# Performance work log

Measured on AMD Instinct MI355X. Metric: run time of the kernel, lower is better.

Reference implementation:

```python
import jax, jax.numpy as jnp
import numpy as np

DIM = 1024
NUM_HEADS = 16
HEAD_DIM = DIM // NUM_HEADS


def setup_inputs() -> dict:
    key = jax.random.key(0)
    k1, k2, k3 = jax.random.split(key, 3)
    x = jax.random.normal(k1, (4, 1024, DIM), dtype=jnp.float32)
    # match nn.Linear init scale roughly: small weights
    Wqkv = jax.random.normal(k2, (3 * DIM, DIM), dtype=jnp.float32) * (1.0 / np.sqrt(DIM))
    Wproj = jax.random.normal(k3, (DIM, DIM), dtype=jnp.float32) * (1.0 / np.sqrt(DIM))
    bproj = jnp.zeros((DIM,), dtype=jnp.float32)
    return {"x": x, "Wqkv": Wqkv, "Wproj": Wproj, "bproj": bproj}


def reference(x, Wqkv, Wproj, bproj):
    bsz, tsz, chans = x.shape
    # fused QKV projection (qkv_bias=False): [B,T,3C]
    qkv = jnp.einsum("btc,oc->bto", x, Wqkv)
    qkv = qkv.reshape(bsz, tsz, 3, NUM_HEADS, HEAD_DIM)
    q = qkv[:, :, 0].transpose(0, 2, 1, 3)  # [B,H,T,D]
    k = qkv[:, :, 1].transpose(0, 2, 1, 3)
    v = qkv[:, :, 2].transpose(0, 2, 1, 3)
    scale = 1.0 / np.sqrt(HEAD_DIM)
    logits = jnp.einsum("bhqd,bhkd->bhqk", q, k) * scale  # [B,H,T,T]
    attn = jax.nn.softmax(logits, axis=-1)
    out = jnp.einsum("bhqk,bhkd->bhqd", attn, v)  # [B,H,T,D]
    out = out.transpose(0, 2, 1, 3).reshape(bsz, tsz, chans)
    return jnp.einsum("btc,oc->bto", out, Wproj) + bproj
```

## Files before the change

### kernel.cpp

```cpp
#include <hip/hip_runtime.h>
#include <hip/hip_bf16.h>

typedef __attribute__((ext_vector_type(8))) short bfrag8;
typedef __attribute__((ext_vector_type(4))) short bfrag4;
typedef __attribute__((ext_vector_type(4))) float floatx4;

typedef unsigned short ushort_t;
typedef unsigned int uint_t;
typedef unsigned long long u64_t;

static __device__ __forceinline__ uint_t pk_bf16(float a, float b) {
    union { __hip_bfloat162 h; uint_t u; } cv;
    cv.h = __float22bfloat162_rn(make_float2(a, b));
    return cv.u;
}

#if __has_builtin(__builtin_amdgcn_mfma_f32_16x16x16_bf16)
static __device__ __forceinline__ floatx4 mfma16(bfrag4 a, bfrag4 b, floatx4 c) {
    return __builtin_amdgcn_mfma_f32_16x16x16_bf16(a, b, c, 0, 0, 0);
}
#elif __has_builtin(__builtin_amdgcn_mfma_f32_16x16x16bf16_1k)
static __device__ __forceinline__ floatx4 mfma16(bfrag4 a, bfrag4 b, floatx4 c) {
    return __builtin_amdgcn_mfma_f32_16x16x16bf16_1k(a, b, c, 0, 0, 0);
}
#else
static __device__ __forceinline__ floatx4 mfma16(bfrag4 a, bfrag4 b, floatx4 c) {
    bfrag8 az = {a[0], 0, a[1], 0, a[2], 0, a[3], 0};
    bfrag8 bz = {b[0], 0, b[1], 0, b[2], 0, b[3], 0};
    return __builtin_amdgcn_mfma_f32_16x16x32_bf16(az, bz, c, 0, 0, 0);
}
#endif

static __device__ __forceinline__ void gl_lds16(const ushort_t* g, ushort_t* l) {
    __builtin_amdgcn_global_load_lds(
        (const __attribute__((address_space(1))) void*)g,
        (__attribute__((address_space(3))) void*)l, 16, 0, 0);
}

__global__ __launch_bounds__(256)
void cvt_all(const float* __restrict__ x, const float* __restrict__ wqkv,
             const float* __restrict__ wproj, ushort_t* __restrict__ xb,
             ushort_t* __restrict__ wqkvb, ushort_t* __restrict__ wprojb) {
    int blk = blockIdx.x;
    const float* src; ushort_t* dst; int base;
    if (blk < 4096)      { src = x;     dst = xb;     base = blk; }
    else if (blk < 7168) { src = wqkv;  dst = wqkvb;  base = blk - 4096; }
    else                 { src = wproj; dst = wprojb; base = blk - 7168; }
    int i = (base * 256 + threadIdx.x) * 4;
    float4 f = *(const float4*)(src + i);
    uint_t lo = pk_bf16(f.x, f.y);
    uint_t hi = pk_bf16(f.z, f.w);
    uint2 u = {lo, hi};
    *(uint2*)(dst + i) = u;
}

__global__ __launch_bounds__(256, 3)
void qkv_gemm(const ushort_t* __restrict__ A, const ushort_t* __restrict__ B,
              ushort_t* __restrict__ qp, ushort_t* __restrict__ kp,
              ushort_t* __restrict__ vTp) {
    const int K = 1024;
    __shared__ ushort_t As[128 * 64];
    __shared__ ushort_t Bs[128 * 64];
    int tid = threadIdx.x;
    int wave = __builtin_amdgcn_readfirstlane(tid >> 6);
    int lane = tid & 63;
    int quad = lane >> 4, l16 = lane & 15;
    int wm = (wave >> 1) * 64, wn = (wave & 1) * 64;
    int m0 = blockIdx.y * 128, n0 = blockIdx.x * 128;

    int rl = lane >> 3;
    int gc = (lane & 7) ^ rl;

    floatx4 acc[4][4] = {};

    const ushort_t* Ag = A + (size_t)m0 * K;
    const ushort_t* Bg = B + (size_t)n0 * K;

    for (int k0 = 0; k0 < K; k0 += 64) {
        __syncthreads();
#pragma unroll
        for (int i = 0; i < 4; i++) {
            int row = wave * 32 + i * 8 + rl;
            gl_lds16(Ag + (size_t)row * K + k0 + gc * 8, &As[(wave * 32 + i * 8) * 64]);
            gl_lds16(Bg + (size_t)row * K + k0 + gc * 8, &Bs[(wave * 32 + i * 8) * 64]);
        }
        __syncthreads();
#pragma unroll
        for (int ks = 0; ks < 2; ks++) {
            bfrag8 af[4], bf[4];
#pragma unroll
            for (int mt = 0; mt < 4; mt++) {
                int r = wm + mt * 16 + l16;
                af[mt] = *(const bfrag8*)&As[r * 64 + ((4 * ks + quad) ^ (r & 7)) * 8];
            }
#pragma unroll
            for (int nt = 0; nt < 4; nt++) {
                int r = wn + nt * 16 + l16;
                bf[nt] = *(const bfrag8*)&Bs[r * 64 + ((4 * ks + quad) ^ (r & 7)) * 8];
            }
#pragma unroll
            for (int mt = 0; mt < 4; mt++)
#pragma unroll
                for (int nt = 0; nt < 4; nt++)
                    acc[mt][nt] = __builtin_amdgcn_mfma_f32_16x16x32_bf16(
                        af[mt], bf[nt], acc[mt][nt], 0, 0, 0);
        }
    }

    int s = n0 >> 10;
    if (s < 2) {
        ushort_t* dst = (s == 0) ? qp : kp;
        float scl = (s == 0) ? 0.125f : 1.0f;
#pragma unroll
        for (int mt = 0; mt < 4; mt++) {
#pragma unroll
            for (int nt = 0; nt < 4; nt++) {
                int o = (n0 & 1023) + wn + nt * 16 + l16;
                int h = o >> 6, d = o & 63;
                uint_t p01 = pk_bf16(acc[mt][nt][0] * scl, acc[mt][nt][1] * scl);
                uint_t p23 = pk_bf16(acc[mt][nt][2] * scl, acc[mt][nt][3] * scl);
                ushort_t pv[4] = {(ushort_t)p01, (ushort_t)(p01 >> 16),
                                  (ushort_t)p23, (ushort_t)(p23 >> 16)};
#pragma unroll
                for (int r = 0; r < 4; r++) {
                    int t = m0 + wm + mt * 16 + quad * 4 + r;
                    int b = t >> 10, tt = t & 1023;
                    dst[((size_t)(b * 16 + h) * 1024 + tt) * 64 + d] = pv[r];
                }
            }
        }
    } else {
#pragma unroll
        for (int mt = 0; mt < 4; mt++) {
            int t = m0 + wm + mt * 16 + quad * 4;
            int b = t >> 10, tt = t & 1023;
#pragma unroll
            for (int nt = 0; nt < 4; nt++) {
                int o = (n0 & 1023) + wn + nt * 16 + l16;
                int h = o >> 6, d = o & 63;
                uint_t p01 = pk_bf16(acc[mt][nt][0], acc[mt][nt][1]);
                uint_t p23 = pk_bf16(acc[mt][nt][2], acc[mt][nt][3]);
                u64_t pk = ((u64_t)p23 << 32) | p01;
                *(u64_t*)&vTp[((size_t)(b * 16 + h) * 64 + d) * 1024 + tt] = pk;
            }
        }
    }
}

__global__ __launch_bounds__(256, 2)
void attn_kernel(const ushort_t* __restrict__ q, const ushort_t* __restrict__ k,
                 const ushort_t* __restrict__ vT, ushort_t* __restrict__ out) {
    int id = blockIdx.x;
    int bh = (id & 7) + ((id >> 6) << 3);
    int qt = (id >> 3) & 7;
    const ushort_t* qb = q + (size_t)bh * 1024 * 64;
    const ushort_t* kb = k + (size_t)bh * 1024 * 64;
    const ushort_t* vtb = vT + (size_t)bh * 64 * 1024;
    int tid = threadIdx.x;
    int wave = __builtin_amdgcn_readfirstlane(tid >> 6);
    int lane = tid & 63;
    int quad = lane >> 4, l16 = lane & 15;
    int q0 = qt * 128 + wave * 32;

    __shared__ ushort_t Ks[128 * 64];
    __shared__ ushort_t VTs[64 * 132];

    int rl = lane >> 3;
    int gc = (lane & 7) ^ rl;

    bfrag8 qf[2][2];
#pragma unroll
    for (int mt = 0; mt < 2; mt++)
#pragma unroll
        for (int ks = 0; ks < 2; ks++)
            qf[mt][ks] = *(const bfrag8*)&qb[(size_t)(q0 + mt * 16 + l16) * 64 + ks * 32 + quad * 8];

    floatx4 oacc[2][4] = {};
    float li[2] = {0.f, 0.f};

    int vd = tid >> 2;
    int vc = tid & 3;

    for (int kt = 0; kt < 8; kt++) {
        uint4 vv[4];
#pragma unroll
        for (int i = 0; i < 4; i++)
            vv[i] = *(const uint4*)&vtb[(size_t)vd * 1024 + kt * 128 + (vc + i * 4) * 8];
        __syncthreads();
#pragma unroll
        for (int i = 0; i < 4; i++) {
            int row = wave * 32 + i * 8 + rl;
            gl_lds16(kb + (size_t)(kt * 128 + row) * 64 + gc * 8, &Ks[(wave * 32 + i * 8) * 64]);
        }
#pragma unroll
        for (int i = 0; i < 4; i++)
            *(uint4*)&VTs[vd * 132 + (vc + i * 4) * 8] = vv[i];
        __syncthreads();

#pragma unroll
        for (int half = 0; half < 2; half++) {
            floatx4 st[2][4] = {};
#pragma unroll
            for (int ks = 0; ks < 2; ks++) {
                bfrag8 kf[4];
#pragma unroll
                for (int tt = 0; tt < 4; tt++) {
                    int r = (half * 4 + tt) * 16 + l16;
                    kf[tt] = *(const bfrag8*)&Ks[r * 64 + ((4 * ks + quad) ^ (r & 7)) * 8];
                }
#pragma unroll
                for (int mt = 0; mt < 2; mt++)
#pragma unroll
                    for (int tt = 0; tt < 4; tt++)
                        st[mt][tt] = __builtin_amdgcn_mfma_f32_16x16x32_bf16(
                            kf[tt], qf[mt][ks], st[mt][tt], 0, 0, 0);
            }

            bfrag4 pf[2][4];
#pragma unroll
            for (int mt = 0; mt < 2; mt++)
#pragma unroll
                for (int tt = 0; tt < 4; tt++) {
                    float p0 = __expf(st[mt][tt][0]);
                    float p1 = __expf(st[mt][tt][1]);
                    float p2 = __expf(st[mt][tt][2]);
                    float p3 = __expf(st[mt][tt][3]);
                    li[mt] += (p0 + p1) + (p2 + p3);
                    union { uint2 u; bfrag4 f; } pk;
                    pk.u.x = pk_bf16(p0, p1);
                    pk.u.y = pk_bf16(p2, p3);
                    pf[mt][tt] = pk.f;
                }

#pragma unroll
            for (int tt = 0; tt < 4; tt++) {
                int keyoff = (half * 4 + tt) * 16;
                bfrag4 vb[4];
#pragma unroll
                for (int nd = 0; nd < 4; nd++)
                    vb[nd] = *(const bfrag4*)&VTs[(nd * 16 + l16) * 132 + keyoff + quad * 4];
#pragma unroll
                for (int mt = 0; mt < 2; mt++)
#pragma unroll
                    for (int nd = 0; nd < 4; nd++)
                        oacc[mt][nd] = mfma16(pf[mt][tt], vb[nd], oacc[mt][nd]);
            }
        }
    }

    float inv[2][4];
#pragma unroll
    for (int mt = 0; mt < 2; mt++) {
        float s0 = li[mt];
        s0 += __shfl_xor(s0, 16);
        s0 += __shfl_xor(s0, 32);
#pragma unroll
        for (int r = 0; r < 4; r++)
            inv[mt][r] = 1.0f / __shfl(s0, quad * 4 + r);
    }

    int b = bh >> 4, h = bh & 15;
#pragma unroll
    for (int mt = 0; mt < 2; mt++)
#pragma unroll
        for (int nd = 0; nd < 4; nd++) {
            uint_t c01 = pk_bf16(oacc[mt][nd][0] * inv[mt][0], oacc[mt][nd][1] * inv[mt][1]);
            uint_t c23 = pk_bf16(oacc[mt][nd][2] * inv[mt][2], oacc[mt][nd][3] * inv[mt][3]);
            ushort_t pv[4] = {(ushort_t)c01, (ushort_t)(c01 >> 16),
                              (ushort_t)c23, (ushort_t)(c23 >> 16)};
#pragma unroll
            for (int r = 0; r < 4; r++) {
                int t = q0 + mt * 16 + quad * 4 + r;
                int c = h * 64 + nd * 16 + l16;
                out[((size_t)(b * 1024 + t)) * 1024 + c] = pv[r];
            }
        }
}

__global__ __launch_bounds__(256, 2)
void proj_gemm(const ushort_t* __restrict__ A, const ushort_t* __restrict__ B,
               const float* __restrict__ bias, float* __restrict__ out) {
    const int K = 1024;
    __shared__ ushort_t As[64 * 64];
    __shared__ ushort_t Bs[128 * 64];
    int tid = threadIdx.x;
    int wave = __builtin_amdgcn_readfirstlane(tid >> 6);
    int lane = tid & 63;
    int quad = lane >> 4, l16 = lane & 15;
    int wm = (wave >> 1) * 32, wn = (wave & 1) * 64;
    int m0 = blockIdx.y * 64, n0 = blockIdx.x * 128;

    int rl = lane >> 3;
    int gc = (lane & 7) ^ rl;

    floatx4 acc[2][4] = {};

    const ushort_t* Ag = A + (size_t)m0 * K;
    const ushort_t* Bg = B + (size_t)n0 * K;

    for (int k0 = 0; k0 < K; k0 += 64) {
        __syncthreads();
#pragma unroll
        for (int i = 0; i < 2; i++) {
            int row = wave * 16 + i * 8 + rl;
            gl_lds16(Ag + (size_t)row * K + k0 + gc * 8, &As[(wave * 16 + i * 8) * 64]);
        }
#pragma unroll
        for (int i = 0; i < 4; i++) {
            int row = wave * 32 + i * 8 + rl;
            gl_lds16(Bg + (size_t)row * K + k0 + gc * 8, &Bs[(wave * 32 + i * 8) * 64]);
        }
        __syncthreads();
#pragma unroll
        for (int ks = 0; ks < 2; ks++) {
            bfrag8 af[2], bf[4];
#pragma unroll
            for (int mt = 0; mt < 2; mt++) {
                int r = wm + mt * 16 + l16;
                af[mt] = *(const bfrag8*)&As[r * 64 + ((4 * ks + quad) ^ (r & 7)) * 8];
            }
#pragma unroll
            for (int nt = 0; nt < 4; nt++) {
                int r = wn + nt * 16 + l16;
                bf[nt] = *(const bfrag8*)&Bs[r * 64 + ((4 * ks + quad) ^ (r & 7)) * 8];
            }
#pragma unroll
            for (int mt = 0; mt < 2; mt++)
#pragma unroll
                for (int nt = 0; nt < 4; nt++)
                    acc[mt][nt] = __builtin_amdgcn_mfma_f32_16x16x32_bf16(
                        af[mt], bf[nt], acc[mt][nt], 0, 0, 0);
        }
    }

#pragma unroll
    for (int mt = 0; mt < 2; mt++) {
#pragma unroll
        for (int nt = 0; nt < 4; nt++) {
            int o = n0 + wn + nt * 16 + l16;
            float bv = bias[o];
#pragma unroll
            for (int r = 0; r < 4; r++) {
                int t = m0 + wm + mt * 16 + quad * 4 + r;
                out[(size_t)t * 1024 + o] = acc[mt][nt][r] + bv;
            }
        }
    }
}

extern "C" void kernel_launch(void* const* d_in, const int* in_sizes, int n_in,
                              void* d_out, int out_size, void* d_ws, size_t ws_size,
                              hipStream_t stream) {
    const float* x     = (const float*)d_in[0];
    const float* Wqkv  = (const float*)d_in[1];
    const float* Wproj = (const float*)d_in[2];
    const float* bproj = (const float*)d_in[3];
    float* out = (float*)d_out;

    char* ws = (char*)d_ws;
    ushort_t* xb     = (ushort_t*)(ws);
    ushort_t* wqkvb  = (ushort_t*)(ws + ((size_t)8 << 20));
    ushort_t* wprojb = (ushort_t*)(ws + ((size_t)14 << 20));
    ushort_t* qp     = (ushort_t*)(ws + ((size_t)16 << 20));
    ushort_t* kp     = (ushort_t*)(ws + ((size_t)24 << 20));
    ushort_t* vTp    = (ushort_t*)(ws + ((size_t)40 << 20));
    ushort_t* attn   = (ushort_t*)(ws + ((size_t)48 << 20));

    cvt_all<<<8192, 256, 0, stream>>>(x, Wqkv, Wproj, xb, wqkvb, wprojb);
    qkv_gemm<<<dim3(24, 32), 256, 0, stream>>>(xb, wqkvb, qp, kp, vTp);
    attn_kernel<<<512, 256, 0, stream>>>(qp, kp, vTp, attn);
    proj_gemm<<<dim3(8, 64), 256, 0, stream>>>(attn, wprojb, bproj, out);
}
```

Measured before the change: 157.9 us.

## Switch GEMMs to 32x32x16 MFMA and add XCD-aware block swizzle

Both the QKV and output-projection GEMMs move from 16x16x32 MFMA tiles to 32x32x16 MFMA tiles. This halves the number of LDS fragment loads per MFMA and uses the denser instruction. The launch grids become 1D, with block indices remapped so that consecutive blocks on the same XCD share M rows for better L2 reuse. The epilogues are rewritten for the 32x32 accumulator layout, and the per-element scatter stores stay in place.

```diff
diff --git a/kernel.cpp b/kernel.cpp
--- a/kernel.cpp
+++ b/kernel.cpp
@@ -4,6 +4,7 @@
 typedef __attribute__((ext_vector_type(8))) short bfrag8;
 typedef __attribute__((ext_vector_type(4))) short bfrag4;
 typedef __attribute__((ext_vector_type(4))) float floatx4;
+typedef __attribute__((ext_vector_type(16))) float floatx16;
 
 typedef unsigned short ushort_t;
 typedef unsigned int uint_t;
@@ -64,14 +65,19 @@
     int tid = threadIdx.x;
     int wave = __builtin_amdgcn_readfirstlane(tid >> 6);
     int lane = tid & 63;
-    int quad = lane >> 4, l16 = lane & 15;
+    int l32 = lane & 31, hi = lane >> 5;
     int wm = (wave >> 1) * 64, wn = (wave & 1) * 64;
-    int m0 = blockIdx.y * 128, n0 = blockIdx.x * 128;
+
+    int id = blockIdx.x;
+    int xcd = id & 7;
+    int s = id >> 3;
+    int m0 = (xcd * 4 + (s & 3)) * 128;
+    int n0 = (s >> 2) * 128;
 
     int rl = lane >> 3;
     int gc = (lane & 7) ^ rl;
 
-    floatx4 acc[4][4] = {};
+    floatx16 acc[2][2] = {};
 
     const ushort_t* Ag = A + (size_t)m0 * K;
     const ushort_t* Bg = B + (size_t)n0 * K;
@@ -86,62 +92,69 @@
         }
         __syncthreads();
 #pragma unroll
-        for (int ks = 0; ks < 2; ks++) {
-            bfrag8 af[4], bf[4];
-#pragma unroll
-            for (int mt = 0; mt < 4; mt++) {
-                int r = wm + mt * 16 + l16;
-                af[mt] = *(const bfrag8*)&As[r * 64 + ((4 * ks + quad) ^ (r & 7)) * 8];
-            }
-#pragma unroll
-            for (int nt = 0; nt < 4; nt++) {
-                int r = wn + nt * 16 + l16;
-                bf[nt] = *(const bfrag8*)&Bs[r * 64 + ((4 * ks + quad) ^ (r & 7)) * 8];
-            }
-#pragma unroll
-            for (int mt = 0; mt < 4; mt++)
-#pragma unroll
-                for (int nt = 0; nt < 4; nt++)
-                    acc[mt][nt] = __builtin_amdgcn_mfma_f32_16x16x32_bf16(
+        for (int kst = 0; kst < 4; kst++) {
+            bfrag8 af[2], bf[2];
+#pragma unroll
+            for (int mt = 0; mt < 2; mt++) {
+                int r = wm + mt * 32 + l32;
+                af[mt] = *(const bfrag8*)&As[r * 64 + ((kst * 2 + hi) ^ (r & 7)) * 8];
+            }
+#pragma unroll
+            for (int nt = 0; nt < 2; nt++) {
+                int r = wn + nt * 32 + l32;
+                bf[nt] = *(const bfrag8*)&Bs[r * 64 + ((kst * 2 + hi) ^ (r & 7)) * 8];
+            }
+#pragma unroll
+            for (int mt = 0; mt < 2; mt++)
+#pragma unroll
+                for (int nt = 0; nt < 2; nt++)
+                    acc[mt][nt] = __builtin_amdgcn_mfma_f32_32x32x16_bf16(
                         af[mt], bf[nt], acc[mt][nt], 0, 0, 0);
         }
     }
 
-    int s = n0 >> 10;
-    if (s < 2) {
-        ushort_t* dst = (s == 0) ? qp : kp;
-        float scl = (s == 0) ? 0.125f : 1.0f;
-#pragma unroll
-        for (int mt = 0; mt < 4; mt++) {
-#pragma unroll
-            for (int nt = 0; nt < 4; nt++) {
-                int o = (n0 & 1023) + wn + nt * 16 + l16;
+    int seg = n0 >> 10;
+    if (seg < 2) {
+        ushort_t* dst = (seg == 0) ? qp : kp;
+        float scl = (seg == 0) ? 0.125f : 1.0f;
+#pragma unroll
+        for (int mt = 0; mt < 2; mt++) {
+#pragma unroll
+            for (int nt = 0; nt < 2; nt++) {
+                int o = (n0 & 1023) + wn + nt * 32 + l32;
                 int h = o >> 6, d = o & 63;
-                uint_t p01 = pk_bf16(acc[mt][nt][0] * scl, acc[mt][nt][1] * scl);
-                uint_t p23 = pk_bf16(acc[mt][nt][2] * scl, acc[mt][nt][3] * scl);
-                ushort_t pv[4] = {(ushort_t)p01, (ushort_t)(p01 >> 16),
-                                  (ushort_t)p23, (ushort_t)(p23 >> 16)};
-#pragma unroll
-                for (int r = 0; r < 4; r++) {
-                    int t = m0 + wm + mt * 16 + quad * 4 + r;
-                    int b = t >> 10, tt = t & 1023;
-                    dst[((size_t)(b * 16 + h) * 1024 + tt) * 64 + d] = pv[r];
+#pragma unroll
+                for (int g = 0; g < 4; g++) {
+                    uint_t p01 = pk_bf16(acc[mt][nt][g * 4 + 0] * scl, acc[mt][nt][g * 4 + 1] * scl);
+                    uint_t p23 = pk_bf16(acc[mt][nt][g * 4 + 2] * scl, acc[mt][nt][g * 4 + 3] * scl);
+                    ushort_t pv[4] = {(ushort_t)p01, (ushort_t)(p01 >> 16),
+                                      (ushort_t)p23, (ushort_t)(p23 >> 16)};
+                    int tbase = m0 + wm + mt * 32 + 8 * g + 4 * hi;
+#pragma unroll
+                    for (int r = 0; r < 4; r++) {
+                        int t = tbase + r;
+                        int b = t >> 10, tt = t & 1023;
+                        dst[((size_t)(b * 16 + h) * 1024 + tt) * 64 + d] = pv[r];
+                    }
                 }
             }
         }
     } else {
 #pragma unroll
-        for (int mt = 0; mt < 4; mt++) {
-            int t = m0 + wm + mt * 16 + quad * 4;
-            int b = t >> 10, tt = t & 1023;
-#pragma unroll
-            for (int nt = 0; nt < 4; nt++) {
-                int o = (n0 & 1023) + wn + nt * 16 + l16;
+        for (int mt = 0; mt < 2; mt++) {
+#pragma unroll
+            for (int nt = 0; nt < 2; nt++) {
+                int o = (n0 & 1023) + wn + nt * 32 + l32;
                 int h = o >> 6, d = o & 63;
-                uint_t p01 = pk_bf16(acc[mt][nt][0], acc[mt][nt][1]);
-                uint_t p23 = pk_bf16(acc[mt][nt][2], acc[mt][nt][3]);
-                u64_t pk = ((u64_t)p23 << 32) | p01;
-                *(u64_t*)&vTp[((size_t)(b * 16 + h) * 64 + d) * 1024 + tt] = pk;
+#pragma unroll
+                for (int g = 0; g < 4; g++) {
+                    int tbase = m0 + wm + mt * 32 + 8 * g + 4 * hi;
+                    int b = tbase >> 10, tt = tbase & 1023;
+                    uint_t p01 = pk_bf16(acc[mt][nt][g * 4 + 0], acc[mt][nt][g * 4 + 1]);
+                    uint_t p23 = pk_bf16(acc[mt][nt][g * 4 + 2], acc[mt][nt][g * 4 + 3]);
+                    u64_t pk = ((u64_t)p23 << 32) | p01;
+                    *(u64_t*)&vTp[((size_t)(b * 16 + h) * 64 + d) * 1024 + tt] = pk;
+                }
             }
         }
     }
@@ -286,14 +299,19 @@
     int tid = threadIdx.x;
     int wave = __builtin_amdgcn_readfirstlane(tid >> 6);
     int lane = tid & 63;
-    int quad = lane >> 4, l16 = lane & 15;
+    int l32 = lane & 31, hi = lane >> 5;
     int wm = (wave >> 1) * 32, wn = (wave & 1) * 64;
-    int m0 = blockIdx.y * 64, n0 = blockIdx.x * 128;
+
+    int id = blockIdx.x;
+    int xcd = id & 7;
+    int s = id >> 3;
+    int m0 = (xcd * 8 + (s & 7)) * 64;
+    int n0 = (s >> 3) * 128;
 
     int rl = lane >> 3;
     int gc = (lane & 7) ^ rl;
 
-    floatx4 acc[2][4] = {};
+    floatx16 acc[2] = {};
 
     const ushort_t* Ag = A + (size_t)m0 * K;
     const ushort_t* Bg = B + (size_t)n0 * K;
@@ -312,38 +330,33 @@
         }
         __syncthreads();
 #pragma unroll
-        for (int ks = 0; ks < 2; ks++) {
-            bfrag8 af[2], bf[4];
-#pragma unroll
-            for (int mt = 0; mt < 2; mt++) {
-                int r = wm + mt * 16 + l16;
-                af[mt] = *(const bfrag8*)&As[r * 64 + ((4 * ks + quad) ^ (r & 7)) * 8];
-            }
-#pragma unroll
-            for (int nt = 0; nt < 4; nt++) {
-                int r = wn + nt * 16 + l16;
-                bf[nt] = *(const bfrag8*)&Bs[r * 64 + ((4 * ks + quad) ^ (r & 7)) * 8];
-            }
-#pragma unroll
-            for (int mt = 0; mt < 2; mt++)
-#pragma unroll
-                for (int nt = 0; nt < 4; nt++)
-                    acc[mt][nt] = __builtin_amdgcn_mfma_f32_16x16x32_bf16(
-                        af[mt], bf[nt], acc[mt][nt], 0, 0, 0);
-        }
-    }
-
-#pragma unroll
-    for (int mt = 0; mt < 2; mt++) {
-#pragma unroll
-        for (int nt = 0; nt < 4; nt++) {
-            int o = n0 + wn + nt * 16 + l16;
-            float bv = bias[o];
-#pragma unroll
-            for (int r = 0; r < 4; r++) {
-                int t = m0 + wm + mt * 16 + quad * 4 + r;
-                out[(size_t)t * 1024 + o] = acc[mt][nt][r] + bv;
-            }
+        for (int kst = 0; kst < 4; kst++) {
+            bfrag8 af, bf[2];
+            {
+                int r = wm + l32;
+                af = *(const bfrag8*)&As[r * 64 + ((kst * 2 + hi) ^ (r & 7)) * 8];
+            }
+#pragma unroll
+            for (int nt = 0; nt < 2; nt++) {
+                int r = wn + nt * 32 + l32;
+                bf[nt] = *(const bfrag8*)&Bs[r * 64 + ((kst * 2 + hi) ^ (r & 7)) * 8];
+            }
+#pragma unroll
+            for (int nt = 0; nt < 2; nt++)
+                acc[nt] = __builtin_amdgcn_mfma_f32_32x32x16_bf16(af, bf[nt], acc[nt], 0, 0, 0);
+        }
+    }
+
+#pragma unroll
+    for (int nt = 0; nt < 2; nt++) {
+        int o = n0 + wn + nt * 32 + l32;
+        float bv = bias[o];
+#pragma unroll
+        for (int g = 0; g < 4; g++) {
+            int tbase = m0 + wm + 8 * g + 4 * hi;
+#pragma unroll
+            for (int r = 0; r < 4; r++)
+                out[(size_t)(tbase + r) * 1024 + o] = acc[nt][g * 4 + r] + bv;
         }
     }
 }
@@ -367,7 +380,7 @@
     ushort_t* attn   = (ushort_t*)(ws + ((size_t)48 << 20));
 
     cvt_all<<<8192, 256, 0, stream>>>(x, Wqkv, Wproj, xb, wqkvb, wprojb);
-    qkv_gemm<<<dim3(24, 32), 256, 0, stream>>>(xb, wqkvb, qp, kp, vTp);
+    qkv_gemm<<<768, 256, 0, stream>>>(xb, wqkvb, qp, kp, vTp);
     attn_kernel<<<512, 256, 0, stream>>>(qp, kp, vTp, attn);
-    proj_gemm<<<dim3(8, 64), 256, 0, stream>>>(attn, wprojb, bproj, out);
-}
+    proj_gemm<<<512, 256, 0, stream>>>(attn, wprojb, bproj, out);
+}
```

Result: slower. 162.8 us (+3.1%).
